# Performance work log

Hardware: AMD Instinct MI355X
Metric: run time of the kernel (lower is better)

Reference implementation:

```python
import jax, jax.numpy as jnp
import numpy as np

B, C, H, W = 1, 256, 64, 64
K_DIM, V_DIM, HEADS = 64, 64, 8


def setup_inputs() -> dict:
    key = jax.random.key(0)
    ks = jax.random.split(key, 13)
    s = lambda i, shape: jax.random.normal(ks[i], shape, dtype=jnp.float32) * 0.05
    return {
        "x": s(0, (B, C, H, W)),
        # low-rank bottleneck projections (bias=False), torch Linear weight is [out,in]
        "wq1": s(1, (K_DIM // 2, C)),
        "wk1": s(2, (K_DIM // 2, C)),
        "wv1": s(3, (V_DIM // 2, C)),
        # expansion to per-head dims (bias=False)
        "wq2": s(4, (K_DIM * HEADS, K_DIM // 2)),
        "wk2": s(5, (K_DIM * HEADS, K_DIM // 2)),
        "wv2": s(6, (V_DIM * HEADS, V_DIM // 2)),
        # output projection (with bias)
        "wo": s(7, (C, V_DIM * HEADS)),
        "bo": s(8, (C,)),
        # depthwise 3x3 conv (groups=C): [C,1,3,3]
        "w_dw": s(9, (C, 1, 3, 3)),
        "b_dw": s(10, (C,)),
        # 1x1 gate conv
        "w_gate": s(11, (C, C, 1, 1)),
        "b_gate": s(12, (C,)),
    }


def reference(x, wq1, wk1, wv1, wq2, wk2, wv2, wo, bo, w_dw, b_dw, w_gate, b_gate):
    B_, C_, H_, W_ = x.shape
    N = H_ * W_
    t = x.transpose(0, 2, 3, 1).reshape(B_, N, C_)  # [B, N, C]
    # low-rank then expansion: Linear(x) = x @ W.T
    q = (t @ wq1.T) @ wq2.T  # [B, N, HEADS*K_DIM]
    k = (t @ wk1.T) @ wk2.T
    v = (t @ wv1.T) @ wv2.T
    q = q.reshape(B_, N, HEADS, K_DIM).transpose(0, 2, 1, 3)  # [B,h,N,dk]
    k = k.reshape(B_, N, HEADS, K_DIM).transpose(0, 2, 1, 3)
    v = v.reshape(B_, N, HEADS, V_DIM).transpose(0, 2, 1, 3)
    attn = jnp.einsum('bhnd,bhmd->bhnm', q, k) / jnp.sqrt(jnp.float32(K_DIM))
    attn = jax.nn.softmax(attn, axis=-1)
    out = jnp.einsum('bhnm,bhmd->bhnd', attn, v)  # [B,h,N,dv]
    out = out.transpose(0, 2, 1, 3).reshape(B_, N, HEADS * V_DIM)
    out = out @ wo.T + bo  # [B, N, C]
    out = out.reshape(B_, H_, W_, C_).transpose(0, 3, 1, 2)  # NCHW
    dn = ('NCHW', 'OIHW', 'NCHW')
    out = jax.lax.conv_general_dilated(out, w_dw, (1, 1), 'SAME', dimension_numbers=dn,
                                       feature_group_count=C_) + b_dw[None, :, None, None]
    gate = jax.nn.sigmoid(
        jax.lax.conv_general_dilated(out, w_gate, (1, 1), 'SAME', dimension_numbers=dn)
        + b_gate[None, :, None, None])
    return out * gate
```

## Files before the change

kernel.cpp:

```cpp
#include <hip/hip_runtime.h>

typedef __bf16 bf16;
typedef __bf16 bf16x4 __attribute__((ext_vector_type(4)));
typedef __bf16 bf16x8 __attribute__((ext_vector_type(8)));
typedef float f32x4 __attribute__((ext_vector_type(4)));

#define MFMA16(a, b, c) __builtin_amdgcn_mfma_f32_16x16x32_bf16((a), (b), (c), 0, 0, 0)

__device__ inline float fexp2(float x) {
    float r;
    asm("v_exp_f32 %0, %1" : "=v"(r) : "v"(x));
    return r;
}

__global__ void k_pre(const float* __restrict__ x, bf16* __restrict__ xt,
                      const float* __restrict__ wq1, const float* __restrict__ wk1,
                      const float* __restrict__ wv1, const float* __restrict__ wq2,
                      const float* __restrict__ wk2, const float* __restrict__ wv2,
                      const float* __restrict__ wo, const float* __restrict__ wg,
                      bf16* __restrict__ Wq, bf16* __restrict__ Wk, bf16* __restrict__ Wv,
                      bf16* __restrict__ wo_bf, bf16* __restrict__ wg_bf) {
    __shared__ float tile[64][68];
    const int bx = blockIdx.x;
    if (bx < 256) {
        const int t = threadIdx.x;
        const int c0 = (bx & 3) * 64;
        const int n0 = (bx >> 2) * 64;
        {
            const int cr = t >> 4, nc = (t & 15) * 4;
#pragma unroll
            for (int i = 0; i < 4; ++i) {
                const float4 v = *(const float4*)(x + (size_t)(c0 + cr + i * 16) * 4096 + n0 + nc);
                tile[cr + i * 16][nc + 0] = v.x;
                tile[cr + i * 16][nc + 1] = v.y;
                tile[cr + i * 16][nc + 2] = v.z;
                tile[cr + i * 16][nc + 3] = v.w;
            }
        }
        __syncthreads();
        const int n = t >> 2, cc = (t & 3) * 16;
        bf16x8 o0, o1;
#pragma unroll
        for (int j = 0; j < 8; ++j) o0[j] = (bf16)tile[cc + j][n];
#pragma unroll
        for (int j = 0; j < 8; ++j) o1[j] = (bf16)tile[cc + 8 + j][n];
        bf16* dst = xt + (size_t)(n0 + n) * 256 + c0 + cc;
        *(bf16x8*)dst = o0;
        *(bf16x8*)(dst + 8) = o1;
    } else {
        int t = (bx - 256) * 256 + threadIdx.x;
        if (t < 393216) {
            int which = t >> 17;
            int rem = t & 131071;
            int o = rem >> 8, c = rem & 255;
            const float* w1 = which == 0 ? wq1 : which == 1 ? wk1 : wv1;
            const float* w2 = which == 0 ? wq2 : which == 1 ? wk2 : wv2;
            float acc = 0.f;
#pragma unroll
            for (int j = 0; j < 32; ++j) acc += w2[o * 32 + j] * w1[j * 256 + c];
            bf16* W = which == 0 ? Wq : which == 1 ? Wk : Wv;
            W[o * 256 + c] = (bf16)acc;
        } else if (t < 524288) {
            int idx = t - 393216;
            wo_bf[idx] = (bf16)wo[idx];
        } else if (t < 589824) {
            int idx = t - 524288;
            wg_bf[idx] = (bf16)wg[idx];
        }
    }
}

template <int MODE>
__device__ __forceinline__ void gemm_body(const bf16* __restrict__ A, const bf16* __restrict__ B,
                                          int K, float scale, void* __restrict__ outp,
                                          int bx, int by) {
    const int lane = threadIdx.x & 63;
    const int w = threadIdx.x >> 6;
    const int i0 = by * 128 + w * 32;
    const int j0 = bx * 64;
    const int lrow = lane & 15;
    const int lk = (lane >> 4) * 8;

    f32x4 acc[2][4];
#pragma unroll
    for (int a = 0; a < 2; ++a)
#pragma unroll
        for (int b = 0; b < 4; ++b) acc[a][b] = (f32x4){0.f, 0.f, 0.f, 0.f};

    for (int k0 = 0; k0 < K; k0 += 32) {
        bf16x8 af[2], bfr[4];
#pragma unroll
        for (int qs = 0; qs < 2; ++qs)
            af[qs] = *(const bf16x8*)(A + (size_t)(i0 + qs * 16 + lrow) * K + k0 + lk);
#pragma unroll
        for (int js = 0; js < 4; ++js)
            bfr[js] = *(const bf16x8*)(B + (size_t)(j0 + js * 16 + lrow) * K + k0 + lk);
#pragma unroll
        for (int qs = 0; qs < 2; ++qs)
#pragma unroll
            for (int js = 0; js < 4; ++js)
                acc[qs][js] = MFMA16(af[qs], bfr[js], acc[qs][js]);
    }

    const int rbase = (lane >> 4) * 4;
#pragma unroll
    for (int qs = 0; qs < 2; ++qs)
#pragma unroll
        for (int js = 0; js < 4; ++js)
#pragma unroll
            for (int r = 0; r < 4; ++r) {
                int i = i0 + qs * 16 + rbase + r;
                int j = j0 + js * 16 + lrow;
                float v = acc[qs][js][r];
                if (MODE == 0) {
                    ((bf16*)outp)[(size_t)(j >> 6) * (4096 * 64) + (size_t)i * 64 + (j & 63)] =
                        (bf16)(v * scale);
                } else {
                    ((bf16*)outp)[(size_t)i * 4096 + j] = (bf16)v;
                }
            }
}

template <int MODE>
__launch_bounds__(256)
__global__ void k_gemm64(const bf16* __restrict__ A, const bf16* __restrict__ B,
                         int K, void* __restrict__ outp,
                         const float* __restrict__ bias, const float* __restrict__ mul) {
    const int lane = threadIdx.x & 63;
    const int w = threadIdx.x >> 6;
    const int i0 = blockIdx.y * 64 + w * 16;
    const int j0 = blockIdx.x * 64;
    const int lrow = lane & 15;
    const int lk = (lane >> 4) * 8;

    f32x4 acc[4];
#pragma unroll
    for (int b = 0; b < 4; ++b) acc[b] = (f32x4){0.f, 0.f, 0.f, 0.f};

    for (int k0 = 0; k0 < K; k0 += 32) {
        bf16x8 af = *(const bf16x8*)(A + (size_t)(i0 + lrow) * K + k0 + lk);
        bf16x8 bfr[4];
#pragma unroll
        for (int js = 0; js < 4; ++js)
            bfr[js] = *(const bf16x8*)(B + (size_t)(j0 + js * 16 + lrow) * K + k0 + lk);
#pragma unroll
        for (int js = 0; js < 4; ++js)
            acc[js] = MFMA16(af, bfr[js], acc[js]);
    }

    const int rbase = (lane >> 4) * 4;
#pragma unroll
    for (int js = 0; js < 4; ++js)
#pragma unroll
        for (int r = 0; r < 4; ++r) {
            int i = i0 + rbase + r;
            int j = j0 + js * 16 + lrow;
            float v = acc[js][r];
            if (MODE == 2) {
                ((float*)outp)[(size_t)i * 4096 + j] = v + bias[i];
            } else {
                float g2 = v + bias[i];
                float sg = 1.f / (1.f + __expf(-g2));
                ((float*)outp)[(size_t)i * 4096 + j] = mul[(size_t)i * 4096 + j] * sg;
            }
        }
}

__launch_bounds__(256)
__global__ void k_qkv(const bf16* __restrict__ xbf, const bf16* __restrict__ Wq,
                      const bf16* __restrict__ Wk, const bf16* __restrict__ Wv,
                      bf16* __restrict__ q_buf, bf16* __restrict__ k_buf,
                      bf16* __restrict__ vT, float qscale) {
    const int b = blockIdx.x;
    if (b < 256) {
        gemm_body<0>(xbf, Wq, 256, qscale, q_buf, b & 7, b >> 3);
    } else if (b < 512) {
        const int bb = b - 256;
        gemm_body<0>(xbf, Wk, 256, 1.0f, k_buf, bb & 7, bb >> 3);
    } else {
        const int bb = b - 512;
        gemm_body<1>(Wv, xbf, 256, 1.0f, vT, bb & 63, bb >> 6);
    }
}

__launch_bounds__(256)
__global__ void k_attn(const bf16* __restrict__ q, const bf16* __restrict__ k,
                       const bf16* __restrict__ vT, bf16* __restrict__ Opart,
                       float* __restrict__ lpart) {
    __shared__ char kvlds[16384];
    __shared__ char plds[4][4096];
    const int tid = threadIdx.x;
    const int lane = tid & 63;
    const int w = tid >> 6;
    const int split = blockIdx.x >> 8;
    const int h = (blockIdx.x >> 5) & 7;
    const int qt = blockIdx.x & 31;
    const int qbase = qt * 128 + w * 32;
    const int lrow = lane & 15;
    const int g = lane >> 4;
    const int swzr = (lrow & 7) << 4;

    const bf16* qh = q + (size_t)h * 4096 * 64;
    const bf16* kh = k + (size_t)h * 4096 * 64;
    const bf16* vh = vT + (size_t)h * 64 * 4096;
    char* myp = plds[w];
    const char* Kl = kvlds;
    const char* Vl = kvlds + 8192;

    const int isV = tid >> 7;
    const int srow = (tid & 127) >> 1;
    const int shalf = tid & 1;
    const int swzs = (srow & 7) << 4;
    char* ldst = kvlds + isV * 8192 + srow * 128;
    const bf16* sbase = isV ? (vh + (size_t)srow * 4096 + split * 1024 + shalf * 32)
                            : (kh + ((size_t)split * 1024 + srow) * 64 + shalf * 32);
    const size_t sstep = isV ? 64 : 64 * 64;

    bf16x8 bq[2][2];
#pragma unroll
    for (int qs = 0; qs < 2; ++qs)
#pragma unroll
        for (int ks = 0; ks < 2; ++ks)
            bq[qs][ks] = *(const bf16x8*)(qh + (size_t)(qbase + qs * 16 + lrow) * 64 +
                                          ks * 32 + g * 8);

    f32x4 accO[2][4];
    f32x4 l_acc[2];
#pragma unroll
    for (int qs = 0; qs < 2; ++qs) {
#pragma unroll
        for (int ds = 0; ds < 4; ++ds) accO[qs][ds] = (f32x4){0.f, 0.f, 0.f, 0.f};
        l_acc[qs] = (f32x4){0.f, 0.f, 0.f, 0.f};
    }
    const f32x4 zero4 = (f32x4){0.f, 0.f, 0.f, 0.f};
    bf16x8 ones;
#pragma unroll
    for (int i = 0; i < 8; ++i) ones[i] = (bf16)1.0f;

    uint4 r0, r1, r2, r3;
    {
        const bf16* p = sbase;
        r0 = *(const uint4*)(p);
        r1 = *(const uint4*)(p + 8);
        r2 = *(const uint4*)(p + 16);
        r3 = *(const uint4*)(p + 24);
    }

    for (int t = 0; t < 16; ++t) {
        *(uint4*)(ldst + ((shalf * 64 + 0) ^ swzs)) = r0;
        *(uint4*)(ldst + ((shalf * 64 + 16) ^ swzs)) = r1;
        *(uint4*)(ldst + ((shalf * 64 + 32) ^ swzs)) = r2;
        *(uint4*)(ldst + ((shalf * 64 + 48) ^ swzs)) = r3;
        if (t < 15) {
            const bf16* p = sbase + (size_t)(t + 1) * sstep;
            r0 = *(const uint4*)(p);
            r1 = *(const uint4*)(p + 8);
            r2 = *(const uint4*)(p + 16);
            r3 = *(const uint4*)(p + 24);
        }
        __syncthreads();

        f32x4 s[2][4];
        __builtin_amdgcn_s_setprio(1);
        {
            bf16x8 ak[4];
#pragma unroll
            for (int js = 0; js < 4; ++js)
                ak[js] = *(const bf16x8*)(Kl + (js * 16 + lrow) * 128 + ((g * 16) ^ swzr));
#pragma unroll
            for (int qs = 0; qs < 2; ++qs)
#pragma unroll
                for (int js = 0; js < 4; ++js)
                    s[qs][js] = MFMA16(ak[js], bq[qs][0], zero4);
        }
        {
            bf16x8 ak[4];
#pragma unroll
            for (int js = 0; js < 4; ++js)
                ak[js] = *(const bf16x8*)(Kl + (js * 16 + lrow) * 128 + ((64 + g * 16) ^ swzr));
#pragma unroll
            for (int qs = 0; qs < 2; ++qs)
#pragma unroll
                for (int js = 0; js < 4; ++js)
                    s[qs][js] = MFMA16(ak[js], bq[qs][1], s[qs][js]);
        }
        __builtin_amdgcn_s_setprio(0);

#pragma unroll
        for (int qs = 0; qs < 2; ++qs) {
            const int qrow = qs * 16 + lrow;
#pragma unroll
            for (int js = 0; js < 4; ++js) {
                bf16x4 pk;
#pragma unroll
                for (int r = 0; r < 4; ++r) pk[r] = (bf16)fexp2(s[qs][js][r]);
                *(bf16x4*)(myp + ((qrow * 128 + js * 32 + g * 8) ^ swzr)) = pk;
            }
        }

        __builtin_amdgcn_s_setprio(1);
#pragma unroll
        for (int ks2 = 0; ks2 < 2; ++ks2) {
            bf16x8 bv[4];
#pragma unroll
            for (int ds = 0; ds < 4; ++ds)
                bv[ds] = *(const bf16x8*)(Vl + (ds * 16 + lrow) * 128 +
                                          ((ks2 * 64 + g * 16) ^ swzr));
            bf16x8 ap0 = *(const bf16x8*)(myp + ((lrow * 128 + ks2 * 64 + g * 16) ^ swzr));
            bf16x8 ap1 = *(const bf16x8*)(myp + (((16 + lrow) * 128 + ks2 * 64 + g * 16) ^ swzr));
#pragma unroll
            for (int ds = 0; ds < 4; ++ds)
                accO[0][ds] = MFMA16(ap0, bv[ds], accO[0][ds]);
            l_acc[0] = MFMA16(ap0, ones, l_acc[0]);
#pragma unroll
            for (int ds = 0; ds < 4; ++ds)
                accO[1][ds] = MFMA16(ap1, bv[ds], accO[1][ds]);
            l_acc[1] = MFMA16(ap1, ones, l_acc[1]);
        }
        __builtin_amdgcn_s_setprio(0);
        __syncthreads();
    }

#pragma unroll
    for (int qs = 0; qs < 2; ++qs)
#pragma unroll
        for (int ds = 0; ds < 4; ++ds)
#pragma unroll
            for (int r = 0; r < 4; ++r) {
                const int n = qbase + qs * 16 + 4 * g + r;
                Opart[((size_t)split * 4096 + n) * 512 + h * 64 + ds * 16 + lrow] =
                    (bf16)accO[qs][ds][r];
            }
    if (lrow == 0) {
#pragma unroll
        for (int qs = 0; qs < 2; ++qs)
#pragma unroll
            for (int r = 0; r < 4; ++r)
                lpart[((size_t)split * 8 + h) * 4096 + qbase + qs * 16 + 4 * g + r] =
                    l_acc[qs][r];
    }
}

__global__ void k_combine(const bf16* __restrict__ Opart, const float* __restrict__ lpart,
                          bf16* __restrict__ o) {
    const int tid = blockIdx.x * 256 + threadIdx.x;
    const int n = tid >> 6;
    const int c8 = (tid & 63) * 8;
    const int h = c8 >> 6;
    float acc[8] = {0, 0, 0, 0, 0, 0, 0, 0};
    float l = 0.f;
#pragma unroll
    for (int s = 0; s < 4; ++s) {
        const bf16x8 v = *(const bf16x8*)(Opart + ((size_t)s * 4096 + n) * 512 + c8);
#pragma unroll
        for (int j = 0; j < 8; ++j) acc[j] += (float)v[j];
        l += lpart[((size_t)s * 8 + h) * 4096 + n];
    }
    const float inv = 1.f / l;
    bf16x8 ov;
#pragma unroll
    for (int j = 0; j < 8; ++j) ov[j] = (bf16)(acc[j] * inv);
    *(bf16x8*)(o + (size_t)n * 512 + c8) = ov;
}

__global__ void k_dw(const float* __restrict__ y, const float* __restrict__ wdw,
                     const float* __restrict__ bdw, float* __restrict__ dwout,
                     bf16* __restrict__ dwt) {
    int t = blockIdx.x * 256 + threadIdx.x;
    int c = t >> 10, rem = t & 1023;
    int yy = rem >> 4, xx0 = (rem & 15) * 4;
    const float* yc = y + (size_t)c * 4096;
    float w0r[3], w1r[3], w2r[3];
#pragma unroll
    for (int ky = 0; ky < 3; ++ky) {
        w0r[ky] = wdw[c * 9 + ky * 3 + 0];
        w1r[ky] = wdw[c * 9 + ky * 3 + 1];
        w2r[ky] = wdw[c * 9 + ky * 3 + 2];
    }
    float b = bdw[c];
    float acc0 = b, acc1 = b, acc2 = b, acc3 = b;
#pragma unroll
    for (int ky = 0; ky < 3; ++ky) {
        int ry = yy + ky - 1;
        if ((unsigned)ry < 64u) {
            const float* row = yc + ry * 64 + xx0;
            float4 v = *(const float4*)row;
            float left = (xx0 > 0) ? row[-1] : 0.f;
            float right = (xx0 < 60) ? row[4] : 0.f;
            acc0 += w0r[ky] * left + w1r[ky] * v.x + w2r[ky] * v.y;
            acc1 += w0r[ky] * v.x + w1r[ky] * v.y + w2r[ky] * v.z;
            acc2 += w0r[ky] * v.y + w1r[ky] * v.z + w2r[ky] * v.w;
            acc3 += w0r[ky] * v.z + w1r[ky] * v.w + w2r[ky] * right;
        }
    }
    const int n = yy * 64 + xx0;
    *(float4*)(dwout + (size_t)c * 4096 + n) = make_float4(acc0, acc1, acc2, acc3);
    dwt[(size_t)(n + 0) * 256 + c] = (bf16)acc0;
    dwt[(size_t)(n + 1) * 256 + c] = (bf16)acc1;
    dwt[(size_t)(n + 2) * 256 + c] = (bf16)acc2;
    dwt[(size_t)(n + 3) * 256 + c] = (bf16)acc3;
}

extern "C" void kernel_launch(void* const* d_in, const int* in_sizes, int n_in,
                              void* d_out, int out_size, void* d_ws, size_t ws_size,
                              hipStream_t stream) {
    const float* x   = (const float*)d_in[0];
    const float* wq1 = (const float*)d_in[1];
    const float* wk1 = (const float*)d_in[2];
    const float* wv1 = (const float*)d_in[3];
    const float* wq2 = (const float*)d_in[4];
    const float* wk2 = (const float*)d_in[5];
    const float* wv2 = (const float*)d_in[6];
    const float* wo  = (const float*)d_in[7];
    const float* bo  = (const float*)d_in[8];
    const float* wdw = (const float*)d_in[9];
    const float* bdw = (const float*)d_in[10];
    const float* wg  = (const float*)d_in[11];
    const float* bg  = (const float*)d_in[12];

    char* ws = (char*)d_ws;
    size_t off = 0;
    auto alloc = [&](size_t bytes) {
        char* p = ws + off;
        off += (bytes + 255) & ~(size_t)255;
        return p;
    };
    bf16*  q_buf = (bf16*)alloc((size_t)8 * 4096 * 64 * 2);
    bf16*  k_buf = (bf16*)alloc((size_t)8 * 4096 * 64 * 2);
    bf16*  vT    = (bf16*)alloc((size_t)8 * 64 * 4096 * 2);
    bf16*  o_buf = (bf16*)alloc((size_t)4096 * 512 * 2);
    bf16*  wo_bf = (bf16*)alloc((size_t)256 * 512 * 2);
    bf16*  wg_bf = (bf16*)alloc((size_t)256 * 256 * 2);
    char* U = ws + off;
    bf16*  xbf = (bf16*)U;
    bf16*  Wq  = (bf16*)(U + (size_t)2 * 1024 * 1024);
    bf16*  Wk  = (bf16*)(U + (size_t)2 * 1024 * 1024 + 262144);
    bf16*  Wv  = (bf16*)(U + (size_t)2 * 1024 * 1024 + 524288);
    bf16*  Opart = (bf16*)U;
    float* lpart = (float*)(U + (size_t)16 * 1024 * 1024);
    float* ybuf  = (float*)U;
    float* dwout = (float*)(U + (size_t)4 * 1024 * 1024);
    bf16*  dwt   = (bf16*)(U + (size_t)8 * 1024 * 1024);
    (void)ws_size; (void)in_sizes; (void)n_in; (void)out_size;

    const float QSCALE = 0.125f * 1.4426950408889634f;

    k_pre<<<2560, 256, 0, stream>>>(x, xbf, wq1, wk1, wv1, wq2, wk2, wv2, wo, wg,
                                    Wq, Wk, Wv, wo_bf, wg_bf);
    k_qkv<<<768, 256, 0, stream>>>(xbf, Wq, Wk, Wv, q_buf, k_buf, vT, QSCALE);
    k_attn<<<1024, 256, 0, stream>>>(q_buf, k_buf, vT, Opart, lpart);
    k_combine<<<1024, 256, 0, stream>>>(Opart, lpart, o_buf);
    k_gemm64<2><<<dim3(64, 4), 256, 0, stream>>>(wo_bf, o_buf, 512, ybuf, bo, nullptr);
    k_dw<<<1024, 256, 0, stream>>>(ybuf, wdw, bdw, dwout, dwt);
    k_gemm64<3><<<dim3(64, 4), 256, 0, stream>>>(wg_bf, dwt, 256, d_out, bg, dwout);
}
```

Before: 111.7 us.

## Fuse split-K combine into output projection and depthwise conv into gate GEMM

Removes the separate combine kernel by having the output-projection GEMM read the four attention partials directly, sum them, and scale by the inverse softmax denominator while forming its B operand. Also fuses the depthwise 3x3 conv with the 1x1 gate GEMM and sigmoid multiply, staging the conv result in shared memory instead of writing dwout and dwt to global memory. This cuts two launches and several intermediate round trips through global memory. In exchange, each oproj block rereads the partials (four blocks along y reread the same Opart data), and dwgate runs only 256 blocks, each reading weights from global memory.

```diff
diff --git a/kernel.cpp b/kernel.cpp
--- a/kernel.cpp
+++ b/kernel.cpp
@@ -119,51 +119,6 @@
                     ((bf16*)outp)[(size_t)i * 4096 + j] = (bf16)v;
                 }
             }
-}
-
-template <int MODE>
-__launch_bounds__(256)
-__global__ void k_gemm64(const bf16* __restrict__ A, const bf16* __restrict__ B,
-                         int K, void* __restrict__ outp,
-                         const float* __restrict__ bias, const float* __restrict__ mul) {
-    const int lane = threadIdx.x & 63;
-    const int w = threadIdx.x >> 6;
-    const int i0 = blockIdx.y * 64 + w * 16;
-    const int j0 = blockIdx.x * 64;
-    const int lrow = lane & 15;
-    const int lk = (lane >> 4) * 8;
-
-    f32x4 acc[4];
-#pragma unroll
-    for (int b = 0; b < 4; ++b) acc[b] = (f32x4){0.f, 0.f, 0.f, 0.f};
-
-    for (int k0 = 0; k0 < K; k0 += 32) {
-        bf16x8 af = *(const bf16x8*)(A + (size_t)(i0 + lrow) * K + k0 + lk);
-        bf16x8 bfr[4];
-#pragma unroll
-        for (int js = 0; js < 4; ++js)
-            bfr[js] = *(const bf16x8*)(B + (size_t)(j0 + js * 16 + lrow) * K + k0 + lk);
-#pragma unroll
-        for (int js = 0; js < 4; ++js)
-            acc[js] = MFMA16(af, bfr[js], acc[js]);
-    }
-
-    const int rbase = (lane >> 4) * 4;
-#pragma unroll
-    for (int js = 0; js < 4; ++js)
-#pragma unroll
-        for (int r = 0; r < 4; ++r) {
-            int i = i0 + rbase + r;
-            int j = j0 + js * 16 + lrow;
-            float v = acc[js][r];
-            if (MODE == 2) {
-                ((float*)outp)[(size_t)i * 4096 + j] = v + bias[i];
-            } else {
-                float g2 = v + bias[i];
-                float sg = 1.f / (1.f + __expf(-g2));
-                ((float*)outp)[(size_t)i * 4096 + j] = mul[(size_t)i * 4096 + j] * sg;
-            }
-        }
 }
 
 __launch_bounds__(256)
@@ -341,64 +296,142 @@
     }
 }
 
-__global__ void k_combine(const bf16* __restrict__ Opart, const float* __restrict__ lpart,
-                          bf16* __restrict__ o) {
-    const int tid = blockIdx.x * 256 + threadIdx.x;
-    const int n = tid >> 6;
-    const int c8 = (tid & 63) * 8;
-    const int h = c8 >> 6;
-    float acc[8] = {0, 0, 0, 0, 0, 0, 0, 0};
-    float l = 0.f;
-#pragma unroll
-    for (int s = 0; s < 4; ++s) {
-        const bf16x8 v = *(const bf16x8*)(Opart + ((size_t)s * 4096 + n) * 512 + c8);
-#pragma unroll
-        for (int j = 0; j < 8; ++j) acc[j] += (float)v[j];
-        l += lpart[((size_t)s * 8 + h) * 4096 + n];
-    }
-    const float inv = 1.f / l;
-    bf16x8 ov;
-#pragma unroll
-    for (int j = 0; j < 8; ++j) ov[j] = (bf16)(acc[j] * inv);
-    *(bf16x8*)(o + (size_t)n * 512 + c8) = ov;
-}
-
-__global__ void k_dw(const float* __restrict__ y, const float* __restrict__ wdw,
-                     const float* __restrict__ bdw, float* __restrict__ dwout,
-                     bf16* __restrict__ dwt) {
-    int t = blockIdx.x * 256 + threadIdx.x;
-    int c = t >> 10, rem = t & 1023;
-    int yy = rem >> 4, xx0 = (rem & 15) * 4;
-    const float* yc = y + (size_t)c * 4096;
-    float w0r[3], w1r[3], w2r[3];
-#pragma unroll
-    for (int ky = 0; ky < 3; ++ky) {
-        w0r[ky] = wdw[c * 9 + ky * 3 + 0];
-        w1r[ky] = wdw[c * 9 + ky * 3 + 1];
-        w2r[ky] = wdw[c * 9 + ky * 3 + 2];
-    }
-    float b = bdw[c];
-    float acc0 = b, acc1 = b, acc2 = b, acc3 = b;
-#pragma unroll
-    for (int ky = 0; ky < 3; ++ky) {
-        int ry = yy + ky - 1;
-        if ((unsigned)ry < 64u) {
-            const float* row = yc + ry * 64 + xx0;
-            float4 v = *(const float4*)row;
-            float left = (xx0 > 0) ? row[-1] : 0.f;
-            float right = (xx0 < 60) ? row[4] : 0.f;
-            acc0 += w0r[ky] * left + w1r[ky] * v.x + w2r[ky] * v.y;
-            acc1 += w0r[ky] * v.x + w1r[ky] * v.y + w2r[ky] * v.z;
-            acc2 += w0r[ky] * v.y + w1r[ky] * v.z + w2r[ky] * v.w;
-            acc3 += w0r[ky] * v.z + w1r[ky] * v.w + w2r[ky] * right;
-        }
-    }
-    const int n = yy * 64 + xx0;
-    *(float4*)(dwout + (size_t)c * 4096 + n) = make_float4(acc0, acc1, acc2, acc3);
-    dwt[(size_t)(n + 0) * 256 + c] = (bf16)acc0;
-    dwt[(size_t)(n + 1) * 256 + c] = (bf16)acc1;
-    dwt[(size_t)(n + 2) * 256 + c] = (bf16)acc2;
-    dwt[(size_t)(n + 3) * 256 + c] = (bf16)acc3;
+__launch_bounds__(256)
+__global__ void k_oproj(const bf16* __restrict__ wo_bf, const bf16* __restrict__ Opart,
+                        const float* __restrict__ lpart, const float* __restrict__ bo,
+                        float* __restrict__ ybuf) {
+    const int lane = threadIdx.x & 63;
+    const int w = threadIdx.x >> 6;
+    const int i0 = blockIdx.y * 64 + w * 16;
+    const int j0 = blockIdx.x * 64;
+    const int lrow = lane & 15;
+    const int lk = (lane >> 4) * 8;
+
+    float linv[4][8];
+#pragma unroll
+    for (int js = 0; js < 4; ++js) {
+        const int n = j0 + js * 16 + lrow;
+#pragma unroll
+        for (int h = 0; h < 8; ++h) {
+            float l = lpart[(0 * 8 + h) * 4096 + n] + lpart[(1 * 8 + h) * 4096 + n] +
+                      lpart[(2 * 8 + h) * 4096 + n] + lpart[(3 * 8 + h) * 4096 + n];
+            linv[js][h] = 1.f / l;
+        }
+    }
+
+    f32x4 acc[4];
+#pragma unroll
+    for (int b = 0; b < 4; ++b) acc[b] = (f32x4){0.f, 0.f, 0.f, 0.f};
+
+    const size_t SP = (size_t)4096 * 512;
+
+#pragma unroll
+    for (int k0 = 0; k0 < 512; k0 += 32) {
+        const int h = k0 >> 6;
+        bf16x8 af = *(const bf16x8*)(wo_bf + (size_t)(i0 + lrow) * 512 + k0 + lk);
+#pragma unroll
+        for (int js = 0; js < 4; ++js) {
+            const size_t nbase = (size_t)(j0 + js * 16 + lrow) * 512 + k0 + lk;
+            bf16x8 b0 = *(const bf16x8*)(Opart + nbase);
+            bf16x8 b1 = *(const bf16x8*)(Opart + SP + nbase);
+            bf16x8 b2 = *(const bf16x8*)(Opart + 2 * SP + nbase);
+            bf16x8 b3 = *(const bf16x8*)(Opart + 3 * SP + nbase);
+            const float li = linv[js][h];
+            bf16x8 bb;
+#pragma unroll
+            for (int e = 0; e < 8; ++e)
+                bb[e] = (bf16)(((float)b0[e] + (float)b1[e] + (float)b2[e] + (float)b3[e]) * li);
+            acc[js] = MFMA16(af, bb, acc[js]);
+        }
+    }
+
+    const int rbase = (lane >> 4) * 4;
+#pragma unroll
+    for (int js = 0; js < 4; ++js)
+#pragma unroll
+        for (int r = 0; r < 4; ++r) {
+            const int i = i0 + rbase + r;
+            const int j = j0 + js * 16 + lrow;
+            ybuf[(size_t)i * 4096 + j] = acc[js][r] + bo[i];
+        }
+}
+
+__launch_bounds__(256)
+__global__ void k_dwgate(const float* __restrict__ y, const float* __restrict__ wdw,
+                         const float* __restrict__ bdw, const bf16* __restrict__ wg_bf,
+                         const float* __restrict__ bg, float* __restrict__ out) {
+    __shared__ bf16 dwt_s[16][264];
+    __shared__ float acc_s[16][264];
+    const int tid = threadIdx.x;
+    const int n0 = blockIdx.x * 16;
+    const int yy = n0 >> 6;
+    const int xx0 = n0 & 63;
+
+    const int xxq = (tid & 3) * 4;
+    const int gx = xx0 + xxq;
+#pragma unroll
+    for (int iter = 0; iter < 4; ++iter) {
+        const int c = (tid >> 2) + iter * 64;
+        const float* yc = y + (size_t)c * 4096;
+        float w0r[3], w1r[3], w2r[3];
+#pragma unroll
+        for (int ky = 0; ky < 3; ++ky) {
+            w0r[ky] = wdw[c * 9 + ky * 3 + 0];
+            w1r[ky] = wdw[c * 9 + ky * 3 + 1];
+            w2r[ky] = wdw[c * 9 + ky * 3 + 2];
+        }
+        const float b = bdw[c];
+        float a0 = b, a1 = b, a2 = b, a3 = b;
+#pragma unroll
+        for (int ky = 0; ky < 3; ++ky) {
+            const int ry = yy + ky - 1;
+            if ((unsigned)ry < 64u) {
+                const float* row = yc + ry * 64 + gx;
+                const float4 v = *(const float4*)row;
+                const float left = (gx > 0) ? row[-1] : 0.f;
+                const float right = (gx < 60) ? row[4] : 0.f;
+                a0 += w0r[ky] * left + w1r[ky] * v.x + w2r[ky] * v.y;
+                a1 += w0r[ky] * v.x + w1r[ky] * v.y + w2r[ky] * v.z;
+                a2 += w0r[ky] * v.y + w1r[ky] * v.z + w2r[ky] * v.w;
+                a3 += w0r[ky] * v.z + w1r[ky] * v.w + w2r[ky] * right;
+            }
+        }
+        dwt_s[xxq + 0][c] = (bf16)a0; acc_s[xxq + 0][c] = a0;
+        dwt_s[xxq + 1][c] = (bf16)a1; acc_s[xxq + 1][c] = a1;
+        dwt_s[xxq + 2][c] = (bf16)a2; acc_s[xxq + 2][c] = a2;
+        dwt_s[xxq + 3][c] = (bf16)a3; acc_s[xxq + 3][c] = a3;
+    }
+    __syncthreads();
+
+    const int lane = tid & 63;
+    const int w = tid >> 6;
+    const int c0 = w * 64;
+    const int lrow = lane & 15;
+    const int lk = (lane >> 4) * 8;
+
+    f32x4 gacc[4];
+#pragma unroll
+    for (int ai = 0; ai < 4; ++ai) gacc[ai] = (f32x4){0.f, 0.f, 0.f, 0.f};
+#pragma unroll
+    for (int k0 = 0; k0 < 256; k0 += 32) {
+        const bf16x8 bfr = *(const bf16x8*)&dwt_s[lrow][k0 + lk];
+#pragma unroll
+        for (int ai = 0; ai < 4; ++ai) {
+            const bf16x8 af = *(const bf16x8*)(wg_bf + (size_t)(c0 + ai * 16 + lrow) * 256 +
+                                               k0 + lk);
+            gacc[ai] = MFMA16(af, bfr, gacc[ai]);
+        }
+    }
+    const int rbase = (lane >> 4) * 4;
+#pragma unroll
+    for (int ai = 0; ai < 4; ++ai)
+#pragma unroll
+        for (int r = 0; r < 4; ++r) {
+            const int c = c0 + ai * 16 + rbase + r;
+            const float g = gacc[ai][r] + bg[c];
+            const float sg = 1.f / (1.f + __expf(-g));
+            out[(size_t)c * 4096 + n0 + lrow] = acc_s[lrow][c] * sg;
+        }
 }
 
 extern "C" void kernel_launch(void* const* d_in, const int* in_sizes, int n_in,
@@ -428,7 +461,6 @@
     bf16*  q_buf = (bf16*)alloc((size_t)8 * 4096 * 64 * 2);
     bf16*  k_buf = (bf16*)alloc((size_t)8 * 4096 * 64 * 2);
     bf16*  vT    = (bf16*)alloc((size_t)8 * 64 * 4096 * 2);
-    bf16*  o_buf = (bf16*)alloc((size_t)4096 * 512 * 2);
     bf16*  wo_bf = (bf16*)alloc((size_t)256 * 512 * 2);
     bf16*  wg_bf = (bf16*)alloc((size_t)256 * 256 * 2);
     char* U = ws + off;
@@ -438,9 +470,7 @@
     bf16*  Wv  = (bf16*)(U + (size_t)2 * 1024 * 1024 + 524288);
     bf16*  Opart = (bf16*)U;
     float* lpart = (float*)(U + (size_t)16 * 1024 * 1024);
-    float* ybuf  = (float*)U;
-    float* dwout = (float*)(U + (size_t)4 * 1024 * 1024);
-    bf16*  dwt   = (bf16*)(U + (size_t)8 * 1024 * 1024);
+    float* ybuf  = (float*)(U + (size_t)17 * 1024 * 1024);
     (void)ws_size; (void)in_sizes; (void)n_in; (void)out_size;
 
     const float QSCALE = 0.125f * 1.4426950408889634f;
@@ -449,8 +479,6 @@
                                     Wq, Wk, Wv, wo_bf, wg_bf);
     k_qkv<<<768, 256, 0, stream>>>(xbf, Wq, Wk, Wv, q_buf, k_buf, vT, QSCALE);
     k_attn<<<1024, 256, 0, stream>>>(q_buf, k_buf, vT, Opart, lpart);
-    k_combine<<<1024, 256, 0, stream>>>(Opart, lpart, o_buf);
-    k_gemm64<2><<<dim3(64, 4), 256, 0, stream>>>(wo_bf, o_buf, 512, ybuf, bo, nullptr);
-    k_dw<<<1024, 256, 0, stream>>>(ybuf, wdw, bdw, dwout, dwt);
-    k_gemm64<3><<<dim3(64, 4), 256, 0, stream>>>(wg_bf, dwt, 256, d_out, bg, dwout);
-}
+    k_oproj<<<dim3(64, 4), 256, 0, stream>>>(wo_bf, Opart, lpart, bo, ybuf);
+    k_dwgate<<<256, 256, 0, stream>>>(ybuf, wdw, bdw, wg_bf, bg, (float*)d_out);
+}
```

After: 140.6 us. 1.26x slower.
